# Kernel optimization log

Measured on AMD Instinct MI355X. Metric: run time of the kernel, lower is better.

The kernel has to match this reference:

```python
import jax, jax.numpy as jnp
import numpy as np

B, K, D = 8, 256, 256   # batch, num_nodes (== node_embedding_dim), embed dim
ALPHA = 0.2             # LeakyReLU negative slope


def setup_inputs() -> dict:
    key = jax.random.key(0)
    ks = jax.random.split(key, 6)
    x = jax.random.normal(ks[0], (B, K, D), jnp.float32)
    adj = jax.random.randint(ks[1], (B, K, K), 0, 2).astype(jnp.int32)
    # lin: Linear(2*D, D)  -> weight (D, 2D), bias (D,)
    W = jax.random.normal(ks[2], (D, 2 * D), jnp.float32) * (1.0 / np.sqrt(2 * D))
    b_lin = jax.random.normal(ks[3], (D,), jnp.float32) * 0.02
    # attention vector a: (D, 1) in torch; use (D,) here
    a = jax.random.normal(ks[4], (D,), jnp.float32) * (1.414 / np.sqrt(D))
    # per-pair bias (num_nodes, num_nodes); zeros-init in torch, small randn for grad testing
    bias = jax.random.normal(ks[5], (K, K), jnp.float32) * 0.01
    return {"x": x, "adj": adj, "W": W, "b_lin": b_lin, "a": a, "bias": bias}


def reference(x, adj, W, b_lin, a, bias):
    # x: (B, K, D) -> transpose to (B, D, K); with K == D the 'nodes' axis is axis 1.
    v = jnp.swapaxes(x, 1, 2)                      # (B, N, F) with N = D, F = K
    residual = v                                   # residual_proj is Identity (use_gatv2)
    # GATv2: lin([v_i || v_j]) = W1 @ v_i + W2 @ v_j + b  (split W along input dim)
    W1, W2 = W[:, :K], W[:, K:]                    # each (D, K)
    left = jnp.einsum('bnf,df->bnd', v, W1)        # (B, N, D)
    right = jnp.einsum('bnf,df->bnd', v, W2)       # (B, N, D)
    pre = left[:, :, None, :] + right[:, None, :, :] + b_lin   # (B, N, N, D)
    h = jnp.where(pre > 0, pre, ALPHA * pre)       # LeakyReLU
    e = jnp.einsum('bijd,d->bij', h, a)            # (B, N, N)
    e = e + bias                                   # use_bias
    neg_inf = jnp.float32(-jnp.inf)
    e = jnp.where(adj == 0, neg_inf, e)            # masked_fill
    all_inf = jnp.all(e == neg_inf, axis=2, keepdims=True)
    e = jnp.where(all_inf, jnp.float32(0.0), e)    # rows fully masked -> uniform attn
    attn = jax.nn.softmax(e, axis=2)               # dropout inactive (eval / p=0)
    out = jax.nn.sigmoid(attn @ v) + residual      # (B, N, F)
    return jnp.swapaxes(out, 1, 2)                 # back to (B, K, D)
```

## Files before the change

kernel.cpp:

```cpp
#include <hip/hip_runtime.h>
#include <hip/hip_bf16.h>
#include <math.h>

#define BB 8
#define BS 65536

typedef __attribute__((ext_vector_type(8))) short short8v;
typedef __attribute__((ext_vector_type(4))) float f32x4;
typedef unsigned short u16;
typedef unsigned int u32;
typedef __attribute__((address_space(1))) const void gv_t;
typedef __attribute__((address_space(3))) void lv_t;

__device__ __forceinline__ u16 f2bf(float v) {
  __hip_bfloat16 h = __float2bfloat16(v);
  return *reinterpret_cast<u16*>(&h);
}

__device__ __forceinline__ short8v frag(const u16* lds, int rb, int sk,
                                        int lane) {
  int r = rb * 16 + (lane & 15);
  int c = sk * 4 + (lane >> 4);
  int cs = c ^ (r & 7);
  return *(const short8v*)(lds + r * 64 + cs * 8);
}

__device__ __forceinline__ void stage_g32(const u16* __restrict__ g, int row0,
                                          int stride, int k0, u16* lds,
                                          int tid) {
  int r = tid >> 3, c = tid & 7;
  int cs = c ^ (r & 7);
  const u16* src = g + (size_t)(row0 + r) * stride + k0 + cs * 8;
  u16* dst = lds + (size_t)(tid & ~63) * 8;
  __builtin_amdgcn_global_load_lds((gv_t*)src, (lv_t*)dst, 16, 0, 0);
}

__global__ __launch_bounds__(256) void d1_proj(
    const float* __restrict__ x, const float* __restrict__ W,
    const float* __restrict__ b_lin, const float* __restrict__ a,
    float* __restrict__ L2p, u32* __restrict__ R2p) {
  __shared__ float xf[64][33];
  __shared__ u16 XT[32 * 64], B1[32 * 64], B2[32 * 64];
  const int bk = blockIdx.x, tid = threadIdx.x;
  const int b = bk & 7, t = bk >> 3;
  const int n0 = (t >> 3) * 32, dd0 = (t & 7) * 32;
  const int lane = tid & 63, wid = tid >> 6;
  const int nh = wid >> 1, dh = wid & 1;
  const float* xb = x + (size_t)b * BS;

  const int r8 = tid >> 5, c32 = tid & 31;
  const int rw = tid >> 3, cw = tid & 7;

  f32x4 accL = f32x4{0.f, 0.f, 0.f, 0.f};
  f32x4 accR = f32x4{0.f, 0.f, 0.f, 0.f};

  for (int ks = 0; ks < 4; ++ks) {
    float xr[8];
#pragma unroll
    for (int it = 0; it < 8; ++it)
      xr[it] = xb[(size_t)(ks * 64 + it * 8 + r8) * 256 + n0 + c32];
    float4 wa0 = *(const float4*)&W[(size_t)(dd0 + rw) * 512 + ks * 64 + cw * 8];
    float4 wa1 = *(const float4*)&W[(size_t)(dd0 + rw) * 512 + ks * 64 + cw * 8 + 4];
    float4 wb0 = *(const float4*)&W[(size_t)(dd0 + rw) * 512 + 256 + ks * 64 + cw * 8];
    float4 wb1 = *(const float4*)&W[(size_t)(dd0 + rw) * 512 + 256 + ks * 64 + cw * 8 + 4];
#pragma unroll
    for (int it = 0; it < 8; ++it) xf[it * 8 + r8][c32] = xr[it];
    __syncthreads();
    {
      u16 o[8];
#pragma unroll
      for (int e = 0; e < 8; ++e) o[e] = f2bf(xf[cw * 8 + e][rw]);
      *(short8v*)&XT[rw * 64 + ((cw ^ (rw & 7)) * 8)] = *(const short8v*)o;
      u16 o1[8] = {f2bf(wa0.x), f2bf(wa0.y), f2bf(wa0.z), f2bf(wa0.w),
                   f2bf(wa1.x), f2bf(wa1.y), f2bf(wa1.z), f2bf(wa1.w)};
      *(short8v*)&B1[rw * 64 + ((cw ^ (rw & 7)) * 8)] = *(const short8v*)o1;
      u16 o2[8] = {f2bf(wb0.x), f2bf(wb0.y), f2bf(wb0.z), f2bf(wb0.w),
                   f2bf(wb1.x), f2bf(wb1.y), f2bf(wb1.z), f2bf(wb1.w)};
      *(short8v*)&B2[rw * 64 + ((cw ^ (rw & 7)) * 8)] = *(const short8v*)o2;
    }
    __syncthreads();
#pragma unroll
    for (int sk = 0; sk < 2; ++sk) {
      short8v xa = frag(XT, nh, sk, lane);
      short8v w1 = frag(B1, dh, sk, lane);
      short8v w2 = frag(B2, dh, sk, lane);
      accL = __builtin_amdgcn_mfma_f32_16x16x32_bf16(xa, w1, accL, 0, 0, 0);
      accR = __builtin_amdgcn_mfma_f32_16x16x32_bf16(w2, xa, accR, 0, 0, 0);
    }
  }

  {
    int ddc = dd0 + dh * 16 + (lane & 15);
    float c2 = fabsf(0.4f * a[ddc]);
    float bl = b_lin[ddc];
    int nr = n0 + nh * 16 + ((lane >> 4) << 2);
#pragma unroll
    for (int q = 0; q < 4; ++q)
      L2p[(size_t)b * BS + (size_t)(nr + q) * 256 + ddc] = c2 * (accL[q] + bl);
  }
  {
    int nc = n0 + nh * 16 + (lane & 15);
    int ddr = dd0 + dh * 16 + ((lane >> 4) << 2);
    float r0 = fabsf(0.4f * a[ddr + 0]) * accR[0];
    float r1 = fabsf(0.4f * a[ddr + 1]) * accR[1];
    float r2 = fabsf(0.4f * a[ddr + 2]) * accR[2];
    float r3 = fabsf(0.4f * a[ddr + 3]) * accR[3];
    u32 p01 = (u32)f2bf(r0) | ((u32)f2bf(r1) << 16);
    u32 p23 = (u32)f2bf(r2) | ((u32)f2bf(r3) << 16);
    u32* Rp = R2p + (size_t)b * 32768;
    Rp[(size_t)(ddr >> 1) * 256 + nc] = p01;
    Rp[(size_t)((ddr >> 1) + 1) * 256 + nc] = p23;
  }
}

__global__ __launch_bounds__(512) void d2_scores(
    const u32* __restrict__ R2p, const float* __restrict__ L2p,
    const float* __restrict__ a, const int* __restrict__ adj,
    const float* __restrict__ bias, u16* __restrict__ attnh) {
  __shared__ float4 Lq[2][256];
  __shared__ float2 sS2[128];
  __shared__ float redm[8][4], reds[8][4];
  const int t = threadIdx.x, j = t & 255, ih = t >> 8;
  const int bk = blockIdx.x, b = bk & 7, i0 = (bk >> 3) * 8;
  const u32* Rb = R2p + (size_t)b * 32768;

  int adjv[4];
  float biasv[4];
#pragma unroll
  for (int ii = 0; ii < 4; ++ii) {
    int row = i0 + ih * 4 + ii;
    adjv[ii] = adj[(size_t)b * BS + (size_t)row * 256 + j];
    biasv[ii] = bias[row * 256 + j];
  }
  {
    const float* Lb = L2p + (size_t)b * BS + (size_t)(i0 + ih * 4) * 256;
    Lq[ih][j] = make_float4(Lb[j], Lb[256 + j], Lb[512 + j], Lb[768 + j]);
    if (t < 128) {
      float2 av = *(const float2*)&a[2 * t];
      sS2[t] = make_float2(av.x >= 0.f ? 1.f : -1.f, av.y >= 0.f ? 1.f : -1.f);
    }
  }
  __syncthreads();

  float e0 = 0.f, e1 = 0.f, e2 = 0.f, e3 = 0.f, srj = 0.f;
#pragma unroll 8
  for (int d2 = 0; d2 < 128; ++d2) {
    u32 u = Rb[d2 * 256 + j];
    float rv0 = __uint_as_float(u << 16);
    float rv1 = __uint_as_float(u & 0xffff0000u);
    float2 ss = sS2[d2];
    float4 lq0 = Lq[ih][2 * d2];
    float4 lq1 = Lq[ih][2 * d2 + 1];
    srj = fmaf(ss.x, rv0, srj);
    srj = fmaf(ss.y, rv1, srj);
    e0 = fmaf(ss.x, fabsf(lq0.x + rv0), e0);
    e1 = fmaf(ss.x, fabsf(lq0.y + rv0), e1);
    e2 = fmaf(ss.x, fabsf(lq0.z + rv0), e2);
    e3 = fmaf(ss.x, fabsf(lq0.w + rv0), e3);
    e0 = fmaf(ss.y, fabsf(lq1.x + rv1), e0);
    e1 = fmaf(ss.y, fabsf(lq1.y + rv1), e1);
    e2 = fmaf(ss.y, fabsf(lq1.z + rv1), e2);
    e3 = fmaf(ss.y, fabsf(lq1.w + rv1), e3);
  }

  float ev[4] = {e0, e1, e2, e3};
  const float sbase = 1.5f * srj;
  const float NEG_INF = -__builtin_inff();
#pragma unroll
  for (int ii = 0; ii < 4; ++ii) {
    ev[ii] += sbase + biasv[ii];
    ev[ii] = (adjv[ii] == 0) ? NEG_INF : ev[ii];
  }
  const int wid = t >> 6, lane = t & 63, wb = ih * 4;
#pragma unroll
  for (int ii = 0; ii < 4; ++ii) {
    float v = ev[ii];
#pragma unroll
    for (int off = 32; off >= 1; off >>= 1) v = fmaxf(v, __shfl_xor(v, off, 64));
    if (lane == 0) redm[wid][ii] = v;
  }
  __syncthreads();
  float p4[4];
#pragma unroll
  for (int ii = 0; ii < 4; ++ii) {
    float m = fmaxf(fmaxf(redm[wb][ii], redm[wb + 1][ii]),
                    fmaxf(redm[wb + 2][ii], redm[wb + 3][ii]));
    p4[ii] = (m == NEG_INF) ? 1.f : __expf(ev[ii] - m);
  }
#pragma unroll
  for (int ii = 0; ii < 4; ++ii) {
    float v = p4[ii];
#pragma unroll
    for (int off = 32; off >= 1; off >>= 1) v += __shfl_xor(v, off, 64);
    if (lane == 0) reds[wid][ii] = v;
  }
  __syncthreads();
#pragma unroll
  for (int ii = 0; ii < 4; ++ii) {
    float ssum = reds[wb][ii] + reds[wb + 1][ii] + reds[wb + 2][ii] +
                 reds[wb + 3][ii];
    attnh[(size_t)b * BS + (size_t)(i0 + ih * 4 + ii) * 256 + j] =
        f2bf(p4[ii] / ssum);
  }
}

__global__ __launch_bounds__(256) void d3_out(const u16* __restrict__ attnh,
                                              const float* __restrict__ x,
                                              float* __restrict__ out) {
  __shared__ u16 At[32 * 64], Bt[32 * 64];
  const int bk = blockIdx.x, tid = threadIdx.x;
  const int b = bk & 7, t = bk >> 3;
  const int f0 = (t >> 3) * 32, i0 = (t & 7) * 32;
  const int lane = tid & 63, wid = tid >> 6;
  const int fh = wid >> 1, ih2 = wid & 1;
  const float* Ax = x + (size_t)b * BS;
  const u16* Bb = attnh + (size_t)b * BS;
  const int rw = tid >> 3, cw = tid & 7;

  f32x4 acc = f32x4{0.f, 0.f, 0.f, 0.f};
  for (int ks = 0; ks < 4; ++ks) {
    stage_g32(Bb, i0, 256, ks * 64, Bt, tid);
    {
      const float* src = Ax + (size_t)(f0 + rw) * 256 + ks * 64 + cw * 8;
      float4 v0 = *(const float4*)src;
      float4 v1 = *(const float4*)(src + 4);
      u16 o[8] = {f2bf(v0.x), f2bf(v0.y), f2bf(v0.z), f2bf(v0.w),
                  f2bf(v1.x), f2bf(v1.y), f2bf(v1.z), f2bf(v1.w)};
      *(short8v*)&At[rw * 64 + ((cw ^ (rw & 7)) * 8)] = *(const short8v*)o;
    }
    __syncthreads();
#pragma unroll
    for (int sk = 0; sk < 2; ++sk) {
      short8v af = frag(At, fh, sk, lane);
      short8v bf = frag(Bt, ih2, sk, lane);
      acc = __builtin_amdgcn_mfma_f32_16x16x32_bf16(af, bf, acc, 0, 0, 0);
    }
    __syncthreads();
  }

  int col = i0 + ih2 * 16 + (lane & 15);
  int rbase = f0 + fh * 16 + ((lane >> 4) << 2);
#pragma unroll
  for (int q = 0; q < 4; ++q) {
    size_t idx = (size_t)b * BS + (size_t)(rbase + q) * 256 + col;
    float sg = 1.f / (1.f + __expf(-acc[q]));
    out[idx] = sg + x[idx];
  }
}

extern "C" void kernel_launch(void* const* d_in, const int* in_sizes, int n_in,
                              void* d_out, int out_size, void* d_ws,
                              size_t ws_size, hipStream_t stream) {
  const float* x = (const float*)d_in[0];
  const int* adj = (const int*)d_in[1];
  const float* W = (const float*)d_in[2];
  const float* b_lin = (const float*)d_in[3];
  const float* a = (const float*)d_in[4];
  const float* bias = (const float*)d_in[5];
  float* out = (float*)d_out;

  float* L2p = (float*)d_ws;
  u32* R2p = (u32*)(L2p + BB * BS);
  u16* attnh = (u16*)(R2p + BB * 32768);

  d1_proj<<<512, 256, 0, stream>>>(x, W, b_lin, a, L2p, R2p);
  d2_scores<<<256, 512, 0, stream>>>(R2p, L2p, a, adj, bias, attnh);
  d3_out<<<512, 256, 0, stream>>>(attnh, x, out);
}
```

Measured before the change: 28.96 us.

## Fuse softmax scores kernel with attention-times-values output GEMM

Merges the score/softmax kernel and the output matmul kernel so the normalized attention rows stay in shared memory as bf16, padded to 16 rows with zeros, and each block computes its 8 output columns with MFMA directly. This removes the attention round-trip through global memory and one kernel launch. In exchange, every block re-reads and re-converts the full 256x256 x slice of its batch from global memory. Half the MFMA tile is wasted on zero rows, and the output stores write only 8 contiguous floats per row.

New measurement: 33.55 us. 15.8% more time.

```diff
diff --git a/kernel.cpp b/kernel.cpp
--- a/kernel.cpp
+++ b/kernel.cpp
@@ -23,16 +23,6 @@
   int c = sk * 4 + (lane >> 4);
   int cs = c ^ (r & 7);
   return *(const short8v*)(lds + r * 64 + cs * 8);
-}
-
-__device__ __forceinline__ void stage_g32(const u16* __restrict__ g, int row0,
-                                          int stride, int k0, u16* lds,
-                                          int tid) {
-  int r = tid >> 3, c = tid & 7;
-  int cs = c ^ (r & 7);
-  const u16* src = g + (size_t)(row0 + r) * stride + k0 + cs * 8;
-  u16* dst = lds + (size_t)(tid & ~63) * 8;
-  __builtin_amdgcn_global_load_lds((gv_t*)src, (lv_t*)dst, 16, 0, 0);
 }
 
 __global__ __launch_bounds__(256) void d1_proj(
@@ -113,17 +103,23 @@
   }
 }
 
-__global__ __launch_bounds__(512) void d2_scores(
+__global__ __launch_bounds__(512) void d23_fused(
     const u32* __restrict__ R2p, const float* __restrict__ L2p,
     const float* __restrict__ a, const int* __restrict__ adj,
-    const float* __restrict__ bias, u16* __restrict__ attnh) {
+    const float* __restrict__ bias, const float* __restrict__ x,
+    float* __restrict__ out) {
   __shared__ float4 Lq[2][256];
   __shared__ float2 sS2[128];
   __shared__ float redm[8][4], reds[8][4];
+  __shared__ u16 PlB[16][264];
   const int t = threadIdx.x, j = t & 255, ih = t >> 8;
   const int bk = blockIdx.x, b = bk & 7, i0 = (bk >> 3) * 8;
   const u32* Rb = R2p + (size_t)b * 32768;
 
+  {
+    int zr = 8 + (t >> 6), zc = (t & 63) * 4;
+    *(uint2*)&PlB[zr][zc] = make_uint2(0u, 0u);
+  }
   int adjv[4];
   float biasv[4];
 #pragma unroll
@@ -199,52 +195,47 @@
   for (int ii = 0; ii < 4; ++ii) {
     float ssum = reds[wb][ii] + reds[wb + 1][ii] + reds[wb + 2][ii] +
                  reds[wb + 3][ii];
-    attnh[(size_t)b * BS + (size_t)(i0 + ih * 4 + ii) * 256 + j] =
-        f2bf(p4[ii] / ssum);
-  }
-}
-
-__global__ __launch_bounds__(256) void d3_out(const u16* __restrict__ attnh,
-                                              const float* __restrict__ x,
-                                              float* __restrict__ out) {
-  __shared__ u16 At[32 * 64], Bt[32 * 64];
-  const int bk = blockIdx.x, tid = threadIdx.x;
-  const int b = bk & 7, t = bk >> 3;
-  const int f0 = (t >> 3) * 32, i0 = (t & 7) * 32;
-  const int lane = tid & 63, wid = tid >> 6;
-  const int fh = wid >> 1, ih2 = wid & 1;
-  const float* Ax = x + (size_t)b * BS;
-  const u16* Bb = attnh + (size_t)b * BS;
-  const int rw = tid >> 3, cw = tid & 7;
-
-  f32x4 acc = f32x4{0.f, 0.f, 0.f, 0.f};
-  for (int ks = 0; ks < 4; ++ks) {
-    stage_g32(Bb, i0, 256, ks * 64, Bt, tid);
-    {
-      const float* src = Ax + (size_t)(f0 + rw) * 256 + ks * 64 + cw * 8;
-      float4 v0 = *(const float4*)src;
-      float4 v1 = *(const float4*)(src + 4);
-      u16 o[8] = {f2bf(v0.x), f2bf(v0.y), f2bf(v0.z), f2bf(v0.w),
-                  f2bf(v1.x), f2bf(v1.y), f2bf(v1.z), f2bf(v1.w)};
-      *(short8v*)&At[rw * 64 + ((cw ^ (rw & 7)) * 8)] = *(const short8v*)o;
-    }
-    __syncthreads();
-#pragma unroll
-    for (int sk = 0; sk < 2; ++sk) {
-      short8v af = frag(At, fh, sk, lane);
-      short8v bf = frag(Bt, ih2, sk, lane);
-      acc = __builtin_amdgcn_mfma_f32_16x16x32_bf16(af, bf, acc, 0, 0, 0);
-    }
-    __syncthreads();
-  }
-
-  int col = i0 + ih2 * 16 + (lane & 15);
-  int rbase = f0 + fh * 16 + ((lane >> 4) << 2);
-#pragma unroll
-  for (int q = 0; q < 4; ++q) {
-    size_t idx = (size_t)b * BS + (size_t)(rbase + q) * 256 + col;
-    float sg = 1.f / (1.f + __expf(-acc[q]));
-    out[idx] = sg + x[idx];
+    PlB[ih * 4 + ii][j] = f2bf(p4[ii] / ssum);
+  }
+  __syncthreads();
+
+  {
+    const int fw = wid * 32;
+    const float* xb2 = x + (size_t)b * BS;
+    const int r0 = lane & 15, hk = (lane >> 4) * 8;
+    f32x4 acc0 = f32x4{0.f, 0.f, 0.f, 0.f};
+    f32x4 acc1 = f32x4{0.f, 0.f, 0.f, 0.f};
+#pragma unroll
+    for (int step = 0; step < 8; ++step) {
+      int kk = step * 32 + hk;
+      const float* p0 = xb2 + (size_t)(fw + r0) * 256 + kk;
+      const float* p1 = xb2 + (size_t)(fw + r0 + 16) * 256 + kk;
+      float4 a0 = *(const float4*)p0;
+      float4 a1 = *(const float4*)(p0 + 4);
+      float4 c0 = *(const float4*)p1;
+      float4 c1 = *(const float4*)(p1 + 4);
+      u16 oa[8] = {f2bf(a0.x), f2bf(a0.y), f2bf(a0.z), f2bf(a0.w),
+                   f2bf(a1.x), f2bf(a1.y), f2bf(a1.z), f2bf(a1.w)};
+      u16 oc[8] = {f2bf(c0.x), f2bf(c0.y), f2bf(c0.z), f2bf(c0.w),
+                   f2bf(c1.x), f2bf(c1.y), f2bf(c1.z), f2bf(c1.w)};
+      short8v bf = *(const short8v*)&PlB[r0][kk];
+      acc0 = __builtin_amdgcn_mfma_f32_16x16x32_bf16(*(const short8v*)oa, bf,
+                                                     acc0, 0, 0, 0);
+      acc1 = __builtin_amdgcn_mfma_f32_16x16x32_bf16(*(const short8v*)oc, bf,
+                                                     acc1, 0, 0, 0);
+    }
+    int col = lane & 15;
+    if (col < 8) {
+      int i = i0 + col;
+      int fb = fw + ((lane >> 4) << 2);
+#pragma unroll
+      for (int q = 0; q < 4; ++q) {
+        size_t idx0 = (size_t)b * BS + (size_t)(fb + q) * 256 + i;
+        size_t idx1 = (size_t)b * BS + (size_t)(fb + 16 + q) * 256 + i;
+        out[idx0] = 1.f / (1.f + __expf(-acc0[q])) + xb2[(size_t)(fb + q) * 256 + i];
+        out[idx1] = 1.f / (1.f + __expf(-acc1[q])) + xb2[(size_t)(fb + 16 + q) * 256 + i];
+      }
+    }
   }
 }
 
@@ -261,9 +252,7 @@
 
   float* L2p = (float*)d_ws;
   u32* R2p = (u32*)(L2p + BB * BS);
-  u16* attnh = (u16*)(R2p + BB * 32768);
 
   d1_proj<<<512, 256, 0, stream>>>(x, W, b_lin, a, L2p, R2p);
-  d2_scores<<<256, 512, 0, stream>>>(R2p, L2p, a, adj, bias, attnh);
-  d3_out<<<512, 256, 0, stream>>>(attnh, x, out);
-}
+  d23_fused<<<256, 512, 0, stream>>>(R2p, L2p, a, adj, bias, x, out);
+}
```
